# Kernel optimization log

Hardware: AMD Instinct MI355X
Metric: run time of the kernel (lower is better)

The kernel has to match this reference:

```python
import jax, jax.numpy as jnp
import numpy as np

N = 20000      # num nodes
E = 320000     # num edges (before self loops)
D = 512        # d_model
H = 4          # gnn_heads
C = 256        # gnn_hidden_dim (per-head out channels)
L = 4          # gnn_num_layers
B = 16         # number of graphs in batch
NEG_SLOPE = 0.2
LN_EPS = 1e-5


def setup_inputs() -> dict:
    key = jax.random.key(0)
    ks = jax.random.split(key, 10)
    s = 0.05
    return {
        "x": jax.random.normal(ks[0], (N, D), jnp.float32),
        "edge_index": jax.random.randint(ks[1], (2, E), 0, N, dtype=jnp.int32),
        "batch": jnp.sort(jax.random.randint(ks[2], (N,), 0, B, dtype=jnp.int32)),
        "W0": jax.random.normal(ks[3], (D, H * C), jnp.float32) * s,
        "W_rest": jax.random.normal(ks[4], (L - 1, H * C, H * C), jnp.float32) * s,
        "att_src": jax.random.normal(ks[5], (L, H, C), jnp.float32) * s,
        "att_dst": jax.random.normal(ks[6], (L, H, C), jnp.float32) * s,
        "conv_bias": jnp.zeros((L, H * C), jnp.float32),
        "proj_W": jax.random.normal(ks[7], (H * C, D), jnp.float32) * s,
        "proj_b": jnp.zeros((D,), jnp.float32),
        "ln_gamma": jnp.ones((D,), jnp.float32),
        "ln_beta": jnp.zeros((D,), jnp.float32),
    }


def _gat_layer(x, src, dst, W, a_src, a_dst, b):
    # x: [N, F_in] -> h: [N, H, C]
    h = (x @ W).reshape(N, H, C)
    alpha_src = jnp.einsum('nhc,hc->nh', h, a_src)   # [N, H]
    alpha_dst = jnp.einsum('nhc,hc->nh', h, a_dst)   # [N, H]
    e = jax.nn.leaky_relu(alpha_src[src] + alpha_dst[dst], NEG_SLOPE)  # [Etot, H]
    # per-destination softmax (every node has a self loop, so segments nonempty)
    m = jax.ops.segment_max(e, dst, num_segments=N)
    ex = jnp.exp(e - m[dst])
    denom = jax.ops.segment_sum(ex, dst, num_segments=N)
    alpha = ex / (denom[dst] + 1e-16)                # [Etot, H]
    out = jax.ops.segment_sum(alpha[:, :, None] * h[src], dst, num_segments=N)  # [N, H, C]
    return out.reshape(N, H * C) + b


def reference(x, edge_index, batch, W0, W_rest, att_src, att_dst, conv_bias,
              proj_W, proj_b, ln_gamma, ln_beta):
    # add self loops (PyG GATConv default)
    loop = jnp.arange(N, dtype=edge_index.dtype)
    src = jnp.concatenate([edge_index[0], loop])
    dst = jnp.concatenate([edge_index[1], loop])

    h = x
    for l in range(L):
        W = W0 if l == 0 else W_rest[l - 1]
        h = _gat_layer(h, src, dst, W, att_src[l], att_dst[l], conv_bias[l])
        h = jax.nn.relu(h)  # dropout: eval mode -> identity

    # global mean pool over nodes per graph
    sums = jax.ops.segment_sum(h, batch, num_segments=B)           # [B, H*C]
    counts = jax.ops.segment_sum(jnp.ones((N,), h.dtype), batch, num_segments=B)
    pooled = sums / jnp.maximum(counts, 1.0)[:, None]

    out = pooled @ proj_W + proj_b                                 # [B, D]
    mu = out.mean(-1, keepdims=True)
    var = ((out - mu) ** 2).mean(-1, keepdims=True)
    return (out - mu) / jnp.sqrt(var + LN_EPS) * ln_gamma + ln_beta
```

## Files before the change

kernel.cpp:

```cpp
#include <hip/hip_runtime.h>
#include <hip/hip_bf16.h>
#include <hip/hip_fp8.h>
#include <math.h>

#define Nn 20000
#define Ee 320000
#define Dd 512
#define Hh 4
#define Cc 256
#define Ll 4
#define Bb 16
#define HC 1024
#define ETOT (Ee + Nn)
#define NEG_SLOPE 0.2f
#define LN_EPS 1e-5f
#define NBLK ((Nn + 255) / 256)

typedef __attribute__((ext_vector_type(8))) __bf16 bf16x8;
typedef __attribute__((ext_vector_type(4))) __bf16 bf16x4;
typedef __attribute__((ext_vector_type(4))) float f32x4;
typedef __attribute__((ext_vector_type(2))) float f32x2;

__device__ __forceinline__ f32x4 fp8x4_to_f32(unsigned int v) {
#if __has_builtin(__builtin_amdgcn_cvt_pk_f32_fp8)
    f32x2 lo = __builtin_amdgcn_cvt_pk_f32_fp8((int)v, false);
    f32x2 hi = __builtin_amdgcn_cvt_pk_f32_fp8((int)v, true);
    f32x4 r; r[0] = lo[0]; r[1] = lo[1]; r[2] = hi[0]; r[3] = hi[1];
    return r;
#else
    f32x4 r;
    #pragma unroll
    for (int i = 0; i < 4; ++i) {
        __hip_fp8_e4m3 q; q.__x = (v >> (8 * i)) & 0xff;
        r[i] = (float)q;
    }
    return r;
#endif
}

__device__ __forceinline__ unsigned char f32_to_fp8(float f) {
    return __hip_fp8_e4m3(f).__x;
}


__device__ __forceinline__ void decode_edge(const int* ei, int e, int& s, int& d) {
    if (e < Ee) { s = ei[e]; d = ei[Ee + e]; }
    else        { s = e - Ee; d = e - Ee; }
}

__global__ void count_deg_kernel(const int* __restrict__ ei, int* __restrict__ deg) {
    int e = blockIdx.x * blockDim.x + threadIdx.x;
    if (e >= ETOT) return;
    int s, d; decode_edge(ei, e, s, d);
    atomicAdd(&deg[d], 1);
}

__global__ void scan1_kernel(const int* __restrict__ deg, int* __restrict__ tmp,
                             int* __restrict__ bsum) {
    __shared__ int sd[256];
    int tid = threadIdx.x;
    int i = blockIdx.x * 256 + tid;
    sd[tid] = (i < Nn) ? deg[i] : 0;
    __syncthreads();
    for (int off = 1; off < 256; off <<= 1) {
        int t = (tid >= off) ? sd[tid - off] : 0;
        __syncthreads();
        sd[tid] += t;
        __syncthreads();
    }
    if (i < Nn) tmp[i] = sd[tid];
    if (tid == 255) bsum[blockIdx.x] = sd[255];
}

__global__ void scan2_kernel(int* __restrict__ bsum) {
    __shared__ int sd[256];
    int tid = threadIdx.x;
    sd[tid] = (tid < NBLK) ? bsum[tid] : 0;
    __syncthreads();
    for (int off = 1; off < 256; off <<= 1) {
        int t = (tid >= off) ? sd[tid - off] : 0;
        __syncthreads();
        sd[tid] += t;
        __syncthreads();
    }
    if (tid < NBLK) bsum[tid] = sd[tid];
}

__global__ void scan3_kernel(const int* __restrict__ tmp, const int* __restrict__ bsum,
                             const int* __restrict__ deg,
                             int* __restrict__ row_ptr, int* __restrict__ cursor) {
    int i = blockIdx.x * 256 + threadIdx.x;
    if (i >= Nn) return;
    int boff = (blockIdx.x == 0) ? 0 : bsum[blockIdx.x - 1];
    int incl = tmp[i] + boff;
    row_ptr[i + 1] = incl;
    cursor[i] = incl - deg[i];
    if (i == 0) row_ptr[0] = 0;
}

__global__ void scatter_kernel(const int* __restrict__ ei, int* __restrict__ cursor,
                               int* __restrict__ csr_src) {
    int e = blockIdx.x * blockDim.x + threadIdx.x;
    if (e >= ETOT) return;
    int s, d; decode_edge(ei, e, s, d);
    int pos = atomicAdd(&cursor[d], 1);
    csr_src[pos] = s;
}


__global__ void cast_kernel(const float* __restrict__ in, __bf16* __restrict__ out, int n4) {
    int i = blockIdx.x * blockDim.x + threadIdx.x;
    if (i >= n4) return;
    f32x4 v = ((const f32x4*)in)[i];
    bf16x4 o;
    #pragma unroll
    for (int k = 0; k < 4; ++k) o[k] = (__bf16)v[k];
    ((bf16x4*)out)[i] = o;
}

__global__ void transpose_cast_kernel(const float* __restrict__ W, __bf16* __restrict__ WT,
                                      int K, int N) {
    __shared__ float tile[32][33];
    W  += (size_t)blockIdx.z * K * N;
    WT += (size_t)blockIdx.z * K * N;
    int n0 = blockIdx.x * 32, k0 = blockIdx.y * 32;
    for (int i = threadIdx.y; i < 32; i += 8)
        tile[i][threadIdx.x] = W[(size_t)(k0 + i) * N + n0 + threadIdx.x];
    __syncthreads();
    for (int i = threadIdx.y; i < 32; i += 8)
        WT[(size_t)(n0 + i) * K + k0 + threadIdx.x] = (__bf16)tile[threadIdx.x][i];
}


__device__ __forceinline__ void async16(const __bf16* g, __bf16* l) {
    __builtin_amdgcn_global_load_lds((const __attribute__((address_space(1))) void*)g,
                                     (__attribute__((address_space(3))) void*)l,
                                     16, 0, 0);
}

__global__ __launch_bounds__(256) void mfma_gemm_kernel(
    const __bf16* __restrict__ A,
    const __bf16* __restrict__ BT,
    unsigned char* __restrict__ C8,
    const float* __restrict__ att_s,
    const float* __restrict__ att_d,
    float* __restrict__ aprt_s,
    float* __restrict__ aprt_d,
    int M, int K)
{
    int lin = blockIdx.y * 8 + blockIdx.x;
    int rblk = (lin >> 6) * 8 + (lin & 7);
    int cblk = (lin >> 3) & 7;
    int rowBase = rblk * 128, colBase = cblk * 128;
    if (rowBase >= M) return;

    __shared__ __bf16 As[2][128 * 32];
    __shared__ __bf16 Bs[2][128 * 32];
    int tid = threadIdx.x;
    int wave = tid >> 6, lane = tid & 63;
    int m16 = lane & 15, quad = lane >> 4;
    int waveRow = (wave >> 1) * 64, waveCol = (wave & 1) * 64;

    f32x4 acc[4][4] = {};

    int srow = wave * 32 + (lane >> 2);
    int gch0 = (lane & 3) ^ ((srow >> 1) & 3);
    int gch1 = (lane & 3) ^ (((srow + 16) >> 1) & 3);
    int gr0 = rowBase + srow;       if (gr0 >= M) gr0 = M - 1;
    int gr1 = rowBase + srow + 16;  if (gr1 >= M) gr1 = M - 1;
    int ldsOff = srow * 32 + (lane & 3) * 8;

    for (int k0 = 0; k0 < K; k0 += 64) {
        #pragma unroll
        for (int p = 0; p < 2; ++p) {
            int kp = k0 + p * 32;
            async16(A + (size_t)gr0 * K + kp + gch0 * 8, &As[p][ldsOff]);
            async16(A + (size_t)gr1 * K + kp + gch1 * 8, &As[p][ldsOff + 16 * 32]);
            async16(BT + (size_t)(colBase + srow) * K + kp + gch0 * 8, &Bs[p][ldsOff]);
            async16(BT + (size_t)(colBase + srow + 16) * K + kp + gch1 * 8, &Bs[p][ldsOff + 16 * 32]);
        }
        __syncthreads();
        #pragma unroll
        for (int p = 0; p < 2; ++p) {
            bf16x8 af[4], bfr[4];
            #pragma unroll
            for (int i = 0; i < 4; ++i) {
                int row = waveRow + i * 16 + m16;
                af[i] = *(const bf16x8*)&As[p][row * 32 + (quad ^ ((row >> 1) & 3)) * 8];
                int col = waveCol + i * 16 + m16;
                bfr[i] = *(const bf16x8*)&Bs[p][col * 32 + (quad ^ ((col >> 1) & 3)) * 8];
            }
            #pragma unroll
            for (int i = 0; i < 4; ++i)
                #pragma unroll
                for (int j = 0; j < 4; ++j)
                    acc[i][j] = __builtin_amdgcn_mfma_f32_16x16x32_bf16(af[i], bfr[j], acc[i][j], 0, 0, 0);
        }
        __syncthreads();
    }

    int cbase = colBase + waveCol;
    int head = cbase >> 8;
    int part = (cblk & 1) * 2 + (wave & 1);
    float as4[4], ad4[4];
    #pragma unroll
    for (int j = 0; j < 4; ++j) {
        int off = (cbase + j * 16 + m16) & 255;
        as4[j] = att_s[head * 256 + off];
        ad4[j] = att_d[head * 256 + off];
    }

    #pragma unroll
    for (int i = 0; i < 4; ++i) {
        int r0 = rowBase + waveRow + i * 16 + quad * 4;
        #pragma unroll
        for (int r = 0; r < 4; ++r) {
            int row = r0 + r;
            float ps = 0.f, pd = 0.f;
            #pragma unroll
            for (int j = 0; j < 4; ++j) {
                float h = acc[i][j][r];
                ps += h * as4[j];
                pd += h * ad4[j];
                if (row < M)
                    C8[(size_t)row * HC + colBase + waveCol + j * 16 + m16] = f32_to_fp8(h);
            }
            #pragma unroll
            for (int off = 1; off < 16; off <<= 1) {
                ps += __shfl_xor(ps, off);
                pd += __shfl_xor(pd, off);
            }
            if (m16 == 0 && row < M) {
                aprt_s[((size_t)part * M + row) * 4 + head] = ps;
                aprt_d[((size_t)part * M + row) * 4 + head] = pd;
            }
        }
    }
}


__global__ void alpha_sum_kernel(const float* __restrict__ aprt_s,
                                 const float* __restrict__ aprt_d,
                                 float* __restrict__ asrc, float* __restrict__ adst) {
    int n = blockIdx.x * 256 + threadIdx.x;
    if (n >= Nn) return;
    f32x4 s = {0.f, 0.f, 0.f, 0.f}, d = {0.f, 0.f, 0.f, 0.f};
    #pragma unroll
    for (int p = 0; p < 4; ++p) {
        f32x4 vs = ((const f32x4*)aprt_s)[(size_t)p * Nn + n];
        f32x4 vd = ((const f32x4*)aprt_d)[(size_t)p * Nn + n];
        #pragma unroll
        for (int k = 0; k < 4; ++k) { s[k] += vs[k]; d[k] += vd[k]; }
    }
    ((f32x4*)asrc)[n] = s;
    ((f32x4*)adst)[n] = d;
}


__global__ __launch_bounds__(256) void ew_kernel(const float* __restrict__ asrc,
                                                 const float* __restrict__ adst,
                                                 const int* __restrict__ row_ptr,
                                                 const int* __restrict__ csr_src,
                                                 float* __restrict__ ewT,
                                                 float* __restrict__ dinv) {
    int grp = threadIdx.x >> 4, lane16 = threadIdx.x & 15;
    int n = blockIdx.x * 16 + grp;
    if (n >= Nn) return;
    int start = row_ptr[n], end = row_ptr[n + 1];
    f32x4 ad = ((const f32x4*)adst)[n];
    f32x4 d = {0.f, 0.f, 0.f, 0.f};
    for (int e = start + lane16; e < end; e += 16) {
        int s = csr_src[e];
        f32x4 as = ((const f32x4*)asrc)[s];
        #pragma unroll
        for (int k = 0; k < 4; ++k) {
            float z = as[k] + ad[k];
            z = (z > 0.f) ? z : NEG_SLOPE * z;
            float ex = __expf(z);
            ewT[(size_t)k * ETOT + e] = ex;
            d[k] += ex;
        }
    }
    #pragma unroll
    for (int off = 8; off > 0; off >>= 1) {
        #pragma unroll
        for (int k = 0; k < 4; ++k) d[k] += __shfl_xor(d[k], off);
    }
    if (lane16 == 0) {
        f32x4 iv;
        #pragma unroll
        for (int k = 0; k < 4; ++k) iv[k] = 1.f / (d[k] + 1e-16f);
        ((f32x4*)dinv)[n] = iv;
    }
}


__global__ __launch_bounds__(256) void agg_slice_kernel(
    const unsigned char* __restrict__ h8,
    const float* __restrict__ ewT,
    const float* __restrict__ dinv,
    const int* __restrict__ row_ptr,
    const int* __restrict__ csr_src,
    const float* __restrict__ bias_l,
    __bf16* __restrict__ outb)
{
    int slice = blockIdx.x;
    int head = slice >> 1;
    int tid = threadIdx.x;
    int nslot = tid >> 3;
    int ch = tid & 7;
    int n = blockIdx.y * 32 + nslot;

    __shared__ int2 ce_sh[1024];
    __shared__ int  rp_sh[33];

    if (tid < 33) rp_sh[tid] = row_ptr[blockIdx.y * 32 + tid];
    __syncthreads();
    int blk_lo = rp_sh[0], blk_hi = rp_sh[32];
    int start = rp_sh[nslot], end = rp_sh[nslot + 1];

    const unsigned char* hs = h8 + slice * 128 + ch * 16;
    const float* ewh = ewT + (size_t)head * ETOT;
    float acc[16] = {};

    for (int c0 = blk_lo; c0 < blk_hi; c0 += 1024) {
        int c1 = min(c0 + 1024, blk_hi);
        int cnt = c1 - c0;
        for (int i = tid; i < cnt; i += 256) {
            int2 v;
            v.x = csr_src[c0 + i];
            v.y = __float_as_int(ewh[c0 + i]);
            ce_sh[i] = v;
        }
        __syncthreads();
        int lo = max(start, c0), hi = min(end, c1);
        for (int e = lo; e < hi; ++e) {
            int2 v = ce_sh[e - c0];
            float w = __int_as_float(v.y);
            uint4 u = *(const uint4*)(hs + (size_t)v.x * HC);
            f32x4 a0 = fp8x4_to_f32(u.x), a1 = fp8x4_to_f32(u.y);
            f32x4 a2 = fp8x4_to_f32(u.z), a3 = fp8x4_to_f32(u.w);
            #pragma unroll
            for (int k = 0; k < 4; ++k) {
                acc[k]      += w * a0[k];
                acc[k + 4]  += w * a1[k];
                acc[k + 8]  += w * a2[k];
                acc[k + 12] += w * a3[k];
            }
        }
        __syncthreads();
    }

    float inv = dinv[n * 4 + head];
    bf16x8 o0, o1;
    #pragma unroll
    for (int k = 0; k < 8; ++k) {
        o0[k] = (__bf16)fmaxf(acc[k] * inv + bias_l[slice * 128 + ch * 16 + k], 0.f);
        o1[k] = (__bf16)fmaxf(acc[k + 8] * inv + bias_l[slice * 128 + ch * 16 + 8 + k], 0.f);
    }
    *(bf16x8*)(outb + (size_t)n * HC + slice * 128 + ch * 16) = o0;
    *(bf16x8*)(outb + (size_t)n * HC + slice * 128 + ch * 16 + 8) = o1;
}


__device__ __forceinline__ int lower_bound_batch(const int* __restrict__ batch, int val) {
    int lo = 0, hi = Nn;
    while (lo < hi) { int mid = (lo + hi) >> 1; if (batch[mid] < val) lo = mid + 1; else hi = mid; }
    return lo;
}

__global__ void pool_kernel(const __bf16* __restrict__ h2b, const int* __restrict__ batch,
                            float* __restrict__ pooledP) {
    int b = blockIdx.x, part = blockIdx.y;
    int tid = threadIdx.x;
    int start = lower_bound_batch(batch, b);
    int end   = lower_bound_batch(batch, b + 1);
    int len = end - start;
    int chunk = (len + 7) / 8;
    int s0 = start + part * chunk;
    int s1 = min(s0 + chunk, end);
    float acc[4] = {0.f, 0.f, 0.f, 0.f};
    for (int n = s0; n < s1; ++n) {
        bf16x4 v = ((const bf16x4*)(h2b + (size_t)n * HC))[tid];
        #pragma unroll
        for (int k = 0; k < 4; ++k) acc[k] += (float)v[k];
    }
    #pragma unroll
    for (int k = 0; k < 4; ++k)
        pooledP[((size_t)part * Bb + b) * HC + tid * 4 + k] = acc[k];
}


__global__ __launch_bounds__(512) void proj_partial_kernel(const float* __restrict__ pooledP,
                                                           const int* __restrict__ batch,
                                                           const float* __restrict__ projW,
                                                           float* __restrict__ projP) {
    int b = blockIdx.x, part = blockIdx.y;
    int d = threadIdx.x;
    __shared__ float psum[HC];
    int start = lower_bound_batch(batch, b);
    int end   = lower_bound_batch(batch, b + 1);
    float inv = 1.0f / fmaxf((float)(end - start), 1.0f);
    for (int k = d; k < HC; k += 512) {
        float s = 0.f;
        #pragma unroll
        for (int p = 0; p < 8; ++p) s += pooledP[((size_t)p * Bb + b) * HC + k];
        psum[k] = s * inv;
    }
    __syncthreads();
    float acc = 0.f;
    int k0 = part * 128;
    for (int k = k0; k < k0 + 128; ++k)
        acc += psum[k] * projW[(size_t)k * Dd + d];
    projP[((size_t)part * Bb + b) * Dd + d] = acc;
}

__global__ __launch_bounds__(512) void ln_kernel(const float* __restrict__ projP,
                                                 const float* __restrict__ projb,
                                                 const float* __restrict__ gamma,
                                                 const float* __restrict__ beta,
                                                 float* __restrict__ out) {
    int b = blockIdx.x;
    int d = threadIdx.x;
    __shared__ float red[512];
    float o = projb[d];
    #pragma unroll
    for (int p = 0; p < 8; ++p) o += projP[((size_t)p * Bb + b) * Dd + d];
    red[d] = o;
    __syncthreads();
    for (int off = 256; off > 0; off >>= 1) {
        if (d < off) red[d] += red[d + off];
        __syncthreads();
    }
    float mu = red[0] / (float)Dd;
    __syncthreads();
    float df = o - mu;
    red[d] = df * df;
    __syncthreads();
    for (int off = 256; off > 0; off >>= 1) {
        if (d < off) red[d] += red[d + off];
        __syncthreads();
    }
    float var = red[0] / (float)Dd;
    out[b * Dd + d] = df / sqrtf(var + LN_EPS) * gamma[d] + beta[d];
}


extern "C" void kernel_launch(void* const* d_in, const int* in_sizes, int n_in,
                              void* d_out, int out_size, void* d_ws, size_t ws_size,
                              hipStream_t stream) {
    const float* x         = (const float*)d_in[0];
    const int*   ei        = (const int*)d_in[1];
    const int*   batch     = (const int*)d_in[2];
    const float* W0        = (const float*)d_in[3];
    const float* W_rest    = (const float*)d_in[4];
    const float* att_src   = (const float*)d_in[5];
    const float* att_dst   = (const float*)d_in[6];
    const float* conv_bias = (const float*)d_in[7];
    const float* proj_W    = (const float*)d_in[8];
    const float* proj_b    = (const float*)d_in[9];
    const float* ln_gamma  = (const float*)d_in[10];
    const float* ln_beta   = (const float*)d_in[11];
    float* out = (float*)d_out;

    char* ws = (char*)d_ws;
    size_t off = 0;
    auto alloc = [&](size_t bytes) {
        void* p = ws + off;
        off = (off + bytes + 255) & ~(size_t)255;
        return p;
    };
    unsigned char* h8 = (unsigned char*)alloc((size_t)Nn * HC);
    __bf16* h2b     = (__bf16*)alloc((size_t)Nn * HC * 2);
    __bf16* xb      = (__bf16*)alloc((size_t)Nn * Dd * 2);
    __bf16* W0T     = (__bf16*)alloc((size_t)HC * Dd * 2);
    __bf16* WrT     = (__bf16*)alloc((size_t)3 * HC * HC * 2);
    float*  aprt_s  = (float*)alloc((size_t)4 * Nn * Hh * 4);
    float*  aprt_d  = (float*)alloc((size_t)4 * Nn * Hh * 4);
    float*  asrc    = (float*)alloc((size_t)Nn * Hh * 4);
    float*  adst    = (float*)alloc((size_t)Nn * Hh * 4);
    float*  ewT     = (float*)alloc((size_t)Hh * ETOT * 4);
    float*  dinv    = (float*)alloc((size_t)Nn * Hh * 4);
    int*    deg     = (int*)alloc((size_t)Nn * 4);
    int*    tmp     = (int*)alloc((size_t)Nn * 4);
    int*    bsum    = (int*)alloc((size_t)256 * 4);
    int*    row_ptr = (int*)alloc((size_t)(Nn + 1) * 4);
    int*    cursor  = (int*)alloc((size_t)Nn * 4);
    int*    csr_src = (int*)alloc((size_t)ETOT * 4);
    float*  pooledP = (float*)alloc((size_t)8 * Bb * HC * 4);
    float*  projP   = (float*)alloc((size_t)8 * Bb * Dd * 4);
    (void)ws_size; (void)in_sizes; (void)n_in; (void)out_size;

    hipMemsetAsync(deg, 0, (size_t)Nn * 4, stream);
    count_deg_kernel<<<(ETOT + 255) / 256, 256, 0, stream>>>(ei, deg);
    scan1_kernel<<<NBLK, 256, 0, stream>>>(deg, tmp, bsum);
    scan2_kernel<<<1, 256, 0, stream>>>(bsum);
    scan3_kernel<<<NBLK, 256, 0, stream>>>(tmp, bsum, deg, row_ptr, cursor);
    scatter_kernel<<<(ETOT + 255) / 256, 256, 0, stream>>>(ei, cursor, csr_src);

    cast_kernel<<<(Nn * Dd / 4 + 255) / 256, 256, 0, stream>>>(x, xb, Nn * Dd / 4);
    transpose_cast_kernel<<<dim3(HC / 32, Dd / 32, 1), dim3(32, 8), 0, stream>>>(W0, W0T, Dd, HC);
    transpose_cast_kernel<<<dim3(HC / 32, HC / 32, 3), dim3(32, 8), 0, stream>>>(W_rest, WrT, HC, HC);

    dim3 gemm_grid(8, 160);
    for (int l = 0; l < Ll; ++l) {
        const __bf16* Afeat = (l == 0) ? xb : h2b;
        int K = (l == 0) ? Dd : HC;
        const __bf16* BT = (l == 0) ? W0T : (WrT + (size_t)(l - 1) * HC * HC);
        mfma_gemm_kernel<<<gemm_grid, 256, 0, stream>>>(
            Afeat, BT, h8, att_src + l * HC, att_dst + l * HC, aprt_s, aprt_d, Nn, K);
        alpha_sum_kernel<<<NBLK, 256, 0, stream>>>(aprt_s, aprt_d, asrc, adst);
        ew_kernel<<<(Nn + 15) / 16, 256, 0, stream>>>(asrc, adst, row_ptr, csr_src, ewT, dinv);
        agg_slice_kernel<<<dim3(8, Nn / 32), 256, 0, stream>>>(
            h8, ewT, dinv, row_ptr, csr_src, conv_bias + l * HC, h2b);
    }

    pool_kernel<<<dim3(Bb, 8), 256, 0, stream>>>(h2b, batch, pooledP);
    proj_partial_kernel<<<dim3(Bb, 8), 512, 0, stream>>>(pooledP, batch, proj_W, projP);
    ln_kernel<<<Bb, 512, 0, stream>>>(projP, proj_b, ln_gamma, ln_beta, out);
}
```

Before: 629.2 us.

## Balance GAT aggregation by splitting edges evenly across slots with LDS atomics

The per-slice aggregation kernel no longer gives each 8-thread slot one destination node's edge range. Each slot now takes a fixed chunk of 32 edges from the block's edge window. Local destination indices are packed into the high bits of the source index, and partial sums are flushed into a shared-memory accumulator with atomic adds whenever the destination changes. This is meant to remove load imbalance from skewed in-degrees, at the cost of a binary search per edge during staging, LDS atomics, and a larger shared-memory footprint that may lower occupancy.

```diff
diff --git a/kernel.cpp b/kernel.cpp
--- a/kernel.cpp
+++ b/kernel.cpp
@@ -307,56 +307,81 @@
     int slice = blockIdx.x;
     int head = slice >> 1;
     int tid = threadIdx.x;
-    int nslot = tid >> 3;
+    int slot = tid >> 3;
     int ch = tid & 7;
-    int n = blockIdx.y * 32 + nslot;
-
-    __shared__ int2 ce_sh[1024];
-    __shared__ int  rp_sh[33];
+
+    __shared__ int2  ce_sh[1024];
+    __shared__ float acc_sh[32 * 132];
+    __shared__ int   rp_sh[33];
 
     if (tid < 33) rp_sh[tid] = row_ptr[blockIdx.y * 32 + tid];
+    for (int i = tid; i < 32 * 132; i += 256) acc_sh[i] = 0.f;
     __syncthreads();
     int blk_lo = rp_sh[0], blk_hi = rp_sh[32];
-    int start = rp_sh[nslot], end = rp_sh[nslot + 1];
 
     const unsigned char* hs = h8 + slice * 128 + ch * 16;
     const float* ewh = ewT + (size_t)head * ETOT;
-    float acc[16] = {};
 
     for (int c0 = blk_lo; c0 < blk_hi; c0 += 1024) {
         int c1 = min(c0 + 1024, blk_hi);
         int cnt = c1 - c0;
         for (int i = tid; i < cnt; i += 256) {
+            int eg = c0 + i;
+            int lo = 0, hi = 32;
+            while (hi - lo > 1) { int mid = (lo + hi) >> 1; if (rp_sh[mid] <= eg) lo = mid; else hi = mid; }
             int2 v;
-            v.x = csr_src[c0 + i];
-            v.y = __float_as_int(ewh[c0 + i]);
+            v.x = csr_src[eg] | (lo << 20);
+            v.y = __float_as_int(ewh[eg]);
             ce_sh[i] = v;
         }
         __syncthreads();
-        int lo = max(start, c0), hi = min(end, c1);
-        for (int e = lo; e < hi; ++e) {
+        int e0 = c0 + slot * 32;
+        int e1 = min(e0 + 32, c1);
+        float racc[16];
+        #pragma unroll
+        for (int k = 0; k < 16; ++k) racc[k] = 0.f;
+        int curd = -1;
+        for (int e = e0; e < e1; ++e) {
             int2 v = ce_sh[e - c0];
+            int d = v.x >> 20;
+            if (d != curd) {
+                if (curd >= 0) {
+                    float* ap = &acc_sh[curd * 132 + ch * 16];
+                    #pragma unroll
+                    for (int k = 0; k < 16; ++k) { atomicAdd(&ap[k], racc[k]); racc[k] = 0.f; }
+                }
+                curd = d;
+            }
             float w = __int_as_float(v.y);
-            uint4 u = *(const uint4*)(hs + (size_t)v.x * HC);
+            uint4 u = *(const uint4*)(hs + (size_t)(v.x & 0xFFFFF) * HC);
             f32x4 a0 = fp8x4_to_f32(u.x), a1 = fp8x4_to_f32(u.y);
             f32x4 a2 = fp8x4_to_f32(u.z), a3 = fp8x4_to_f32(u.w);
             #pragma unroll
             for (int k = 0; k < 4; ++k) {
-                acc[k]      += w * a0[k];
-                acc[k + 4]  += w * a1[k];
-                acc[k + 8]  += w * a2[k];
-                acc[k + 12] += w * a3[k];
+                racc[k]      += w * a0[k];
+                racc[k + 4]  += w * a1[k];
+                racc[k + 8]  += w * a2[k];
+                racc[k + 12] += w * a3[k];
             }
         }
-        __syncthreads();
-    }
-
+        if (curd >= 0) {
+            float* ap = &acc_sh[curd * 132 + ch * 16];
+            #pragma unroll
+            for (int k = 0; k < 16; ++k) atomicAdd(&ap[k], racc[k]);
+        }
+        __syncthreads();
+    }
+
+    int nslot = tid >> 3;
+    int n = blockIdx.y * 32 + nslot;
     float inv = dinv[n * 4 + head];
     bf16x8 o0, o1;
     #pragma unroll
     for (int k = 0; k < 8; ++k) {
-        o0[k] = (__bf16)fmaxf(acc[k] * inv + bias_l[slice * 128 + ch * 16 + k], 0.f);
-        o1[k] = (__bf16)fmaxf(acc[k + 8] * inv + bias_l[slice * 128 + ch * 16 + 8 + k], 0.f);
+        o0[k] = (__bf16)fmaxf(acc_sh[nslot * 132 + ch * 16 + k] * inv
+                              + bias_l[slice * 128 + ch * 16 + k], 0.f);
+        o1[k] = (__bf16)fmaxf(acc_sh[nslot * 132 + ch * 16 + 8 + k] * inv
+                              + bias_l[slice * 128 + ch * 16 + 8 + k], 0.f);
     }
     *(bf16x8*)(outb + (size_t)n * HC + slice * 128 + ch * 16) = o0;
     *(bf16x8*)(outb + (size_t)n * HC + slice * 128 + ch * 16 + 8) = o1;
```

Measured after the change: 1.177 ms. 87.1% more time.
